# Performance work log

Measured on AMD Instinct MI355X. Metric: run time of the kernel, lower is better.

## Reference

```python
import jax, jax.numpy as jnp
import numpy as np

DN = ('NCHW', 'OIHW', 'NCHW')
BLOB_HW = 16  # hard-coded in make_gaussian_blob_maps

_ENC = [(32, 3), (32, 32), (64, 32), (64, 64), (128, 64), (128, 128), (128, 128)]
_DEC = [(64, 128), (64, 64), (32, 64), (32, 32), (16, 32), (16, 16)]


def _conv(x, w, b, stride):
    y = jax.lax.conv_general_dilated(x, w, (stride, stride), 'SAME', dimension_numbers=DN)
    return y + b[None, :, None, None]


def _tconv(x, w, b):
    # decoder stride-2 stage: 'iteratively doubling the input width'
    y = jax.lax.conv_transpose(x, w, (2, 2), 'SAME', dimension_numbers=DN)
    return y + b[None, :, None, None]


def setup_inputs() -> dict:
    key = jax.random.key(0)
    keys = jax.random.split(key, 1 + 2 * (len(_ENC) + len(_DEC)))
    inp = {'x': jax.random.normal(keys[0], (4, 8, 3, 128, 128), jnp.float32)}
    i = 1
    for j, (o, c) in enumerate(_ENC):
        inp[f'enc_w{j}'] = 0.05 * jax.random.normal(keys[i], (o, c, 3, 3), jnp.float32); i += 1
        inp[f'enc_b{j}'] = 0.05 * jax.random.normal(keys[i], (o,), jnp.float32); i += 1
    for j, (o, c) in enumerate(_DEC):
        inp[f'dec_w{j}'] = 0.05 * jax.random.normal(keys[i], (o, c, 3, 3), jnp.float32); i += 1
        inp[f'dec_b{j}'] = 0.05 * jax.random.normal(keys[i], (o,), jnp.float32); i += 1
    return inp


def _forward(x, enc_w0, enc_b0, enc_w1, enc_b1, enc_w2, enc_b2, enc_w3, enc_b3,
             enc_w4, enc_b4, enc_w5, enc_b5, enc_w6, enc_b6,
             dec_w0, dec_b0, dec_w1, dec_b1, dec_w2, dec_b2,
             dec_w3, dec_b3, dec_w4, dec_b4, dec_w5, dec_b5):
    N, T = x.shape[0], x.shape[1]
    xi = x.reshape((N * T,) + x.shape[2:])  # (B, 3, 128, 128)
    # ---- encoder ----
    h = _conv(xi, enc_w0, enc_b0, 1)                              # Identity act
    h = _conv(h, enc_w1, enc_b1, 1)                               # Identity act
    h = jax.nn.leaky_relu(_conv(h, enc_w2, enc_b2, 2), 0.2)       # 128 -> 64
    h = jax.nn.leaky_relu(_conv(h, enc_w3, enc_b3, 1), 0.2)
    h = jax.nn.leaky_relu(_conv(h, enc_w4, enc_b4, 2), 0.2)       # 64 -> 32
    h = jax.nn.leaky_relu(_conv(h, enc_w5, enc_b5, 1), 0.2)
    R = jax.nn.softplus(_conv(h, enc_w6, enc_b6, 2))              # (B, K, 16, 16)
    B, K, H, W = R.shape
    # ---- keypoint presence: mean over spatial dims ----
    mu = R.sum((2, 3)) / (H * W)                                  # (B, K)
    # ---- normalize_feature_maps: faithful net effect of the in-place loop,
    # which ends up dividing each batch item by the ORIGINAL sum of its LAST map ----
    denom = R[:, K - 1].sum((1, 2))                               # (B,)
    D = R / denom[:, None, None, None]
    # ---- average_feature_maps: spatial-index weighted sum (soft-argmax) ----
    gh = jnp.arange(H, dtype=R.dtype)
    gw = jnp.arange(W, dtype=R.dtype)
    c0 = jnp.einsum('bkhw,h->bk', D, gh)                          # row coord
    c1 = jnp.einsum('bkhw,w->bk', D, gw)                          # col coord
    # ---- gaussian blob maps: mu * exp(-0.5 * ||(u,v) - c||^2), sigma = 1 ----
    u = jnp.arange(BLOB_HW, dtype=R.dtype)[:, None]               # (16, 1)
    v = jnp.arange(BLOB_HW, dtype=R.dtype)[None, :]               # (1, 16)
    d2 = (u[None, None] - c0[:, :, None, None]) ** 2 + (v[None, None] - c1[:, :, None, None]) ** 2
    maps = mu[:, :, None, None] * jnp.exp(-0.5 * d2)              # (B, K, 16, 16)
    # ---- decoder ----
    g = jax.nn.relu(_tconv(maps, dec_w0, dec_b0))                 # 16 -> 32
    g = jax.nn.relu(_conv(g, dec_w1, dec_b1, 1))
    g = jax.nn.relu(_tconv(g, dec_w2, dec_b2))                    # 32 -> 64
    g = jax.nn.relu(_conv(g, dec_w3, dec_b3, 1))
    g = jax.nn.relu(_tconv(g, dec_w4, dec_b4))                    # 64 -> 128
    g = jax.nn.relu(_conv(g, dec_w5, dec_b5, 1))
    return g  # original forward returns the un-reshaped (N*T, C, H, W) tensor


def reference(x, enc_w0, enc_b0, enc_w1, enc_b1, enc_w2, enc_b2, enc_w3, enc_b3,
              enc_w4, enc_b4, enc_w5, enc_b5, enc_w6, enc_b6,
              dec_w0, dec_b0, dec_w1, dec_b1, dec_w2, dec_b2,
              dec_w3, dec_b3, dec_w4, dec_b4, dec_w5, dec_b5):
    return _forward(x, enc_w0, enc_b0, enc_w1, enc_b1, enc_w2, enc_b2, enc_w3, enc_b3,
                    enc_w4, enc_b4, enc_w5, enc_b5, enc_w6, enc_b6,
                    dec_w0, dec_b0, dec_w1, dec_b1, dec_w2, dec_b2,
                    dec_w3, dec_b3, dec_w4, dec_b4, dec_w5, dec_b5)
```

## Files before the change

### kernel.cpp

```cpp
#include <hip/hip_runtime.h>
#include <math.h>


enum { ACT_ID = 0, ACT_LRELU = 1, ACT_SOFTPLUS = 2, ACT_RELU = 3 };

template<int ACT>
__device__ __forceinline__ float act_fn(float x) {
  if (ACT == ACT_LRELU)    return x >= 0.f ? x : 0.2f * x;
  if (ACT == ACT_SOFTPLUS) return fmaxf(x, 0.f) + log1pf(expf(-fabsf(x)));
  if (ACT == ACT_RELU)     return fmaxf(x, 0.f);
  return x;
}

template<int ACT, int NC, int CPT, int CIN>
__global__ __launch_bounds__(256)
void conv_s1(const float* __restrict__ in, const float* __restrict__ w,
             const float* __restrict__ bias, float* __restrict__ out,
             int Cout, int H, int W) {
  const int cogs = Cout / NC;
  const int gx  = blockIdx.x;
  const int cog = gx % cogs;
  const int b   = gx / cogs;
  const int co0 = cog * NC;
  const int Wq  = W / CPT;
  const int items = H * Wq;
  const int item  = blockIdx.y * 256 + threadIdx.x;
  if (item >= items) return;
  const int y  = item / Wq;
  const int x0 = (item - y * Wq) * CPT;

  const int HW = H * W;
  const float* ib = in + (size_t)b * CIN * HW;

  const bool okT = (y > 0), okB = (y < H - 1);
  const bool okL = (x0 > 0), okR = (x0 + CPT < W);
  const int ym = okT ? (y - 1) : 0;
  const int yp = okB ? (y + 1) : 0;
  const int xl = okL ? (x0 - 1) : 0;
  const int xr = okR ? (x0 + CPT) : 0;

  float acc[NC][CPT];
  #pragma unroll
  for (int u = 0; u < NC; ++u)
    #pragma unroll
    for (int q = 0; q < CPT; ++q) acc[u][q] = 0.f;

  #pragma unroll 2
  for (int ci = 0; ci < CIN; ++ci) {
    const float* p = ib + ci * HW;
    const float* wci = w + ((size_t)co0 * CIN + ci) * 9;
    #pragma unroll
    for (int dy = 0; dy < 3; ++dy) {
      const int  ry    = (dy == 0) ? ym : ((dy == 1) ? y : yp);
      const bool okRow = (dy == 0) ? okT : ((dy == 1) ? true : okB);
      const float* r = p + ry * W;
      float v[CPT + 2];
      if (CPT == 4) {
        float  lf = r[xl];
        float4 m  = *(const float4*)(r + x0);
        float  rf = r[xr];
        v[0] = (okRow && okL) ? lf : 0.f;
        v[1] = okRow ? m.x : 0.f;
        v[2] = okRow ? m.y : 0.f;
        v[3] = okRow ? m.z : 0.f;
        v[4] = okRow ? m.w : 0.f;
        v[5] = (okRow && okR) ? rf : 0.f;
      } else if (CPT == 2) {
        float  lf = r[xl];
        float2 m  = *(const float2*)(r + x0);
        float  rf = r[xr];
        v[0] = (okRow && okL) ? lf : 0.f;
        v[1] = okRow ? m.x : 0.f;
        v[2] = okRow ? m.y : 0.f;
        v[3] = (okRow && okR) ? rf : 0.f;
      } else {
        v[0] = (okRow && okL) ? r[xl] : 0.f;
        #pragma unroll
        for (int q = 0; q < CPT; ++q) v[1 + q] = okRow ? r[x0 + q] : 0.f;
        v[CPT + 1] = (okRow && okR) ? r[xr] : 0.f;
      }
      #pragma unroll
      for (int u = 0; u < NC; ++u) {
        const float* wp = wci + u * CIN * 9 + dy * 3;
        const float w0 = wp[0], w1 = wp[1], w2 = wp[2];
        #pragma unroll
        for (int q = 0; q < CPT; ++q)
          acc[u][q] += v[q] * w0 + v[q + 1] * w1 + v[q + 2] * w2;
      }
    }
  }

  #pragma unroll
  for (int u = 0; u < NC; ++u) {
    const float bv = bias[co0 + u];
    float* op = out + ((size_t)(b * Cout + co0 + u) * H + y) * W + x0;
    if (CPT == 4) {
      float4 r4;
      r4.x = act_fn<ACT>(acc[u][0] + bv);
      r4.y = act_fn<ACT>(acc[u][1] + bv);
      r4.z = act_fn<ACT>(acc[u][2] + bv);
      r4.w = act_fn<ACT>(acc[u][3] + bv);
      *(float4*)op = r4;
    } else if (CPT == 2) {
      float2 r2;
      r2.x = act_fn<ACT>(acc[u][0] + bv);
      r2.y = act_fn<ACT>(acc[u][1] + bv);
      *(float2*)op = r2;
    } else {
      #pragma unroll
      for (int q = 0; q < CPT; ++q) op[q] = act_fn<ACT>(acc[u][q] + bv);
    }
  }
}

template<int ACT, int NC, int CPT, int CIN>
__global__ __launch_bounds__(256)
void conv_s2(const float* __restrict__ in, const float* __restrict__ w,
             const float* __restrict__ bias, float* __restrict__ out,
             int Cout, int H, int W) {
  const int Ho = H >> 1, Wo = W >> 1;
  const int cogs = Cout / NC;
  const int gx  = blockIdx.x;
  const int cog = gx % cogs;
  const int b   = gx / cogs;
  const int co0 = cog * NC;
  const int Wq  = Wo / CPT;
  const int items = Ho * Wq;
  const int item  = blockIdx.y * 256 + threadIdx.x;
  if (item >= items) return;
  const int y  = item / Wq;
  const int x0 = (item - y * Wq) * CPT;
  const int ix = 2 * x0;

  const int HW = H * W;
  const float* ib = in + (size_t)b * CIN * HW;

  const int iy0 = 2 * y, iy1 = 2 * y + 1, iy2 = 2 * y + 2;
  const bool okB = (iy2 < H);
  const int iy2c = okB ? iy2 : 0;
  const bool okR = (ix + 2 * CPT < W);
  const int ixr  = okR ? (ix + 2 * CPT) : 0;

  float acc[NC][CPT];
  #pragma unroll
  for (int u = 0; u < NC; ++u)
    #pragma unroll
    for (int q = 0; q < CPT; ++q) acc[u][q] = 0.f;

  #pragma unroll 2
  for (int ci = 0; ci < CIN; ++ci) {
    const float* p = ib + ci * HW;
    const float* wci = w + ((size_t)co0 * CIN + ci) * 9;
    #pragma unroll
    for (int dy = 0; dy < 3; ++dy) {
      const int  ry    = (dy == 0) ? iy0 : ((dy == 1) ? iy1 : iy2c);
      const bool okRow = (dy < 2) || okB;
      const float* r = p + ry * W;
      float v[2 * CPT + 1];
      if (CPT == 4) {
        float4 m0 = *(const float4*)(r + ix);
        float4 m1 = *(const float4*)(r + ix + 4);
        float  rf = r[ixr];
        v[0] = okRow ? m0.x : 0.f; v[1] = okRow ? m0.y : 0.f;
        v[2] = okRow ? m0.z : 0.f; v[3] = okRow ? m0.w : 0.f;
        v[4] = okRow ? m1.x : 0.f; v[5] = okRow ? m1.y : 0.f;
        v[6] = okRow ? m1.z : 0.f; v[7] = okRow ? m1.w : 0.f;
        v[8] = (okRow && okR) ? rf : 0.f;
      } else if (CPT == 2) {
        float4 m0 = *(const float4*)(r + ix);
        float  rf = r[ixr];
        v[0] = okRow ? m0.x : 0.f; v[1] = okRow ? m0.y : 0.f;
        v[2] = okRow ? m0.z : 0.f; v[3] = okRow ? m0.w : 0.f;
        v[4] = (okRow && okR) ? rf : 0.f;
      } else if (CPT == 1) {
        float2 m0 = *(const float2*)(r + ix);
        float  rf = r[ixr];
        v[0] = okRow ? m0.x : 0.f; v[1] = okRow ? m0.y : 0.f;
        v[2] = (okRow && okR) ? rf : 0.f;
      } else {
        #pragma unroll
        for (int q = 0; q < 2 * CPT; ++q) v[q] = okRow ? r[ix + q] : 0.f;
        v[2 * CPT] = (okRow && okR) ? r[ixr] : 0.f;
      }
      #pragma unroll
      for (int u = 0; u < NC; ++u) {
        const float* wp = wci + u * CIN * 9 + dy * 3;
        const float w0 = wp[0], w1 = wp[1], w2 = wp[2];
        #pragma unroll
        for (int q = 0; q < CPT; ++q)
          acc[u][q] += v[2*q] * w0 + v[2*q + 1] * w1 + v[2*q + 2] * w2;
      }
    }
  }

  #pragma unroll
  for (int u = 0; u < NC; ++u) {
    const float bv = bias[co0 + u];
    float* op = out + ((size_t)(b * Cout + co0 + u) * Ho + y) * Wo + x0;
    if (CPT == 4) {
      float4 r4;
      r4.x = act_fn<ACT>(acc[u][0] + bv);
      r4.y = act_fn<ACT>(acc[u][1] + bv);
      r4.z = act_fn<ACT>(acc[u][2] + bv);
      r4.w = act_fn<ACT>(acc[u][3] + bv);
      *(float4*)op = r4;
    } else if (CPT == 2) {
      float2 r2;
      r2.x = act_fn<ACT>(acc[u][0] + bv);
      r2.y = act_fn<ACT>(acc[u][1] + bv);
      *(float2*)op = r2;
    } else {
      #pragma unroll
      for (int q = 0; q < CPT; ++q) op[q] = act_fn<ACT>(acc[u][q] + bv);
    }
  }
}

template<int ACT, int NC, int CIN>
__global__ __launch_bounds__(256)
void tconv(const float* __restrict__ in, const float* __restrict__ w,
           const float* __restrict__ bias, float* __restrict__ out,
           int Cout, int Hin) {
  const int cogs = Cout / NC;
  const int gx  = blockIdx.x;
  const int cog = gx % cogs;
  const int b   = gx / cogs;
  const int co0 = cog * NC;
  const int items = Hin * Hin;
  const int item  = blockIdx.y * 256 + threadIdx.x;
  if (item >= items) return;
  const int i = item / Hin;
  const int j = item - i * Hin;

  const float* ib = in + (size_t)b * CIN * items;
  const bool okT = (i > 0), okL = (j > 0);
  const int im = okT ? i - 1 : 0;
  const int jm = okL ? j - 1 : 0;

  float a00[NC], a01[NC], a10[NC], a11[NC];
  #pragma unroll
  for (int u = 0; u < NC; ++u) { a00[u]=0.f; a01[u]=0.f; a10[u]=0.f; a11[u]=0.f; }

  #pragma unroll 4
  for (int ci = 0; ci < CIN; ++ci) {
    const float* p = ib + ci * items;
    float xtl = p[im*Hin + jm]; xtl = (okT && okL) ? xtl : 0.f;
    float xtr = p[im*Hin + j];  xtr = okT ? xtr : 0.f;
    float xbl = p[i*Hin + jm];  xbl = okL ? xbl : 0.f;
    float xbr = p[i*Hin + j];
    const float* wci = w + ((size_t)co0 * CIN + ci) * 9;
    #pragma unroll
    for (int u = 0; u < NC; ++u) {
      const float* wp = wci + u * CIN * 9;
      const float w00 = wp[0], w01 = wp[1], w02 = wp[2];
      const float w10 = wp[3], w11 = wp[4], w12 = wp[5];
      const float w20 = wp[6], w21 = wp[7], w22 = wp[8];
      a00[u] += xtl*w00 + xtr*w02 + xbl*w20 + xbr*w22;
      a01[u] += xtr*w01 + xbr*w21;
      a10[u] += xbl*w10 + xbr*w12;
      a11[u] += xbr*w11;
    }
  }

  const int Ho = Hin * 2;
  #pragma unroll
  for (int u = 0; u < NC; ++u) {
    const float bv = bias[co0 + u];
    float* op = out + (size_t)(b * Cout + co0 + u) * Ho * Ho + (2*i) * Ho + 2*j;
    float2 t0, t1;
    t0.x = act_fn<ACT>(a00[u] + bv); t0.y = act_fn<ACT>(a01[u] + bv);
    t1.x = act_fn<ACT>(a10[u] + bv); t1.y = act_fn<ACT>(a11[u] + bv);
    *(float2*)op = t0;
    *(float2*)(op + Ho) = t1;
  }
}

__global__ __launch_bounds__(64)
void kp_reduce(const float* __restrict__ R, float* __restrict__ S,
               float* __restrict__ Sh, float* __restrict__ Sw) {
  const int bk = blockIdx.x;
  const int t = threadIdx.x;
  const float* p = R + (size_t)bk * 256;
  float s = 0.f, sh = 0.f, sw = 0.f;
  #pragma unroll
  for (int q = 0; q < 4; ++q) {
    int idx = t + q * 64;
    float v = p[idx];
    s  += v;
    sh += v * (float)(idx >> 4);
    sw += v * (float)(idx & 15);
  }
  #pragma unroll
  for (int off = 32; off > 0; off >>= 1) {
    s  += __shfl_down(s, off);
    sh += __shfl_down(sh, off);
    sw += __shfl_down(sw, off);
  }
  if (t == 0) { S[bk] = s; Sh[bk] = sh; Sw[bk] = sw; }
}

__global__ __launch_bounds__(256)
void kp_maps(const float* __restrict__ S, const float* __restrict__ Sh,
             const float* __restrict__ Sw, float* __restrict__ maps, int K) {
  const int bk = blockIdx.x;
  const int b = bk / K;
  const int t = threadIdx.x;
  const float s   = S[bk];
  const float den = S[b * K + (K - 1)];
  const float mu  = s * (1.0f / 256.0f);
  const float c0  = Sh[bk] / den;
  const float c1  = Sw[bk] / den;
  const float u = (float)(t >> 4);
  const float v = (float)(t & 15);
  const float d2 = (u - c0) * (u - c0) + (v - c1) * (v - c1);
  maps[(size_t)bk * 256 + t] = mu * expf(-0.5f * d2);
}

extern "C" void kernel_launch(void* const* d_in, const int* in_sizes, int n_in,
                              void* d_out, int out_size, void* d_ws, size_t ws_size,
                              hipStream_t stream) {
  const int B = 32;
  const float* x = (const float*)d_in[0];
  const float* ew[7]; const float* eb[7];
  for (int j = 0; j < 7; ++j) { ew[j] = (const float*)d_in[1 + 2*j]; eb[j] = (const float*)d_in[2 + 2*j]; }
  const float* dw[6]; const float* db[6];
  for (int j = 0; j < 6; ++j) { dw[j] = (const float*)d_in[15 + 2*j]; db[j] = (const float*)d_in[16 + 2*j]; }

  float* ws   = (float*)d_ws;
  float* bufA = ws;
  float* bufB = bufA + 16777216;
  float* R    = bufB + 16777216;
  float* maps = R + 1048576;
  float* S    = maps + 1048576;
  float* Sh   = S + 4096;
  float* Sw   = Sh + 4096;
  float* outp = (float*)d_out;

  dim3 blk(256);

  conv_s1<ACT_ID,      8,4,3>  <<<dim3(B*4,  16), blk, 0, stream>>>(x,    ew[0], eb[0], bufA, 32,  128, 128);
  conv_s1<ACT_ID,      8,4,32> <<<dim3(B*4,  16), blk, 0, stream>>>(bufA, ew[1], eb[1], bufB, 32,  128, 128);
  conv_s2<ACT_LRELU,   8,4,32> <<<dim3(B*8,   4), blk, 0, stream>>>(bufB, ew[2], eb[2], bufA, 64,  128, 128);
  conv_s1<ACT_LRELU,   8,4,64> <<<dim3(B*8,   4), blk, 0, stream>>>(bufA, ew[3], eb[3], bufB, 64,  64,  64);
  conv_s2<ACT_LRELU,   8,2,64> <<<dim3(B*16,  2), blk, 0, stream>>>(bufB, ew[4], eb[4], bufA, 128, 64,  64);
  conv_s1<ACT_LRELU,   8,2,128><<<dim3(B*16,  2), blk, 0, stream>>>(bufA, ew[5], eb[5], bufB, 128, 32,  32);
  conv_s2<ACT_SOFTPLUS,4,1,128><<<dim3(B*32,  1), blk, 0, stream>>>(bufB, ew[6], eb[6], R,    128, 32,  32);

  kp_reduce<<<dim3(B*128), dim3(64), 0, stream>>>(R, S, Sh, Sw);
  kp_maps  <<<dim3(B*128), blk, 0, stream>>>(S, Sh, Sw, maps, 128);

  tconv<ACT_RELU,   2,128><<<dim3(B*32,  1), blk, 0, stream>>>(maps, dw[0], db[0], bufA, 64, 16);
  conv_s1<ACT_RELU, 4,2,64><<<dim3(B*16,  2), blk, 0, stream>>>(bufA, dw[1], db[1], bufB, 64, 32, 32);
  tconv<ACT_RELU,   4,64> <<<dim3(B*8,   4), blk, 0, stream>>>(bufB, dw[2], db[2], bufA, 32, 32);
  conv_s1<ACT_RELU, 8,2,32><<<dim3(B*4,   8), blk, 0, stream>>>(bufA, dw[3], db[3], bufB, 32, 64, 64);
  tconv<ACT_RELU,   8,32> <<<dim3(B*2,  16), blk, 0, stream>>>(bufB, dw[4], db[4], bufA, 16, 64);
  conv_s1<ACT_RELU, 8,4,16><<<dim3(B*2,  16), blk, 0, stream>>>(bufA, dw[5], db[5], outp, 16, 128, 128);
}
```

Before: 1.301 ms.

## Compute two output rows per thread in stride-1 convs to reuse input rows

Adds a conv_s1r2 kernel in which each thread produces two adjacent output rows. It loads four input rows per channel instead of three per output row, cutting input loads per output and reusing each loaded row for both outputs. Most stride-1 convs switch to it, several with fewer output channels per block (8 to 4) to keep register pressure and grid size in check. The tconv channel-loop unroll also drops from 4 to 2, and unused CPT branches are removed from the older kernels.

```diff
diff --git a/kernel.cpp b/kernel.cpp
--- a/kernel.cpp
+++ b/kernel.cpp
@@ -10,6 +10,121 @@
   if (ACT == ACT_SOFTPLUS) return fmaxf(x, 0.f) + log1pf(expf(-fabsf(x)));
   if (ACT == ACT_RELU)     return fmaxf(x, 0.f);
   return x;
+}
+
+template<int ACT, int NC, int CPT, int CIN>
+__global__ __launch_bounds__(256)
+void conv_s1r2(const float* __restrict__ in, const float* __restrict__ w,
+               const float* __restrict__ bias, float* __restrict__ out,
+               int Cout, int H, int W) {
+  const int cogs = Cout / NC;
+  const int gx  = blockIdx.x;
+  const int cog = gx % cogs;
+  const int b   = gx / cogs;
+  const int co0 = cog * NC;
+  const int Wq  = W / CPT;
+  const int Hp  = H >> 1;
+  const int items = Hp * Wq;
+  const int item  = blockIdx.y * 256 + threadIdx.x;
+  if (item >= items) return;
+  const int yp = item / Wq;
+  const int x0 = (item - yp * Wq) * CPT;
+  const int y0 = 2 * yp;
+
+  const int HW = H * W;
+  const float* ib = in + (size_t)b * CIN * HW;
+
+  const bool okT = (y0 > 0), okB = (y0 + 2 < H);
+  const bool okL = (x0 > 0), okR = (x0 + CPT < W);
+  const int xl = okL ? (x0 - 1) : 0;
+  const int xr = okR ? (x0 + CPT) : 0;
+
+  float acc[NC][2][CPT];
+  #pragma unroll
+  for (int u = 0; u < NC; ++u)
+    #pragma unroll
+    for (int o = 0; o < 2; ++o)
+      #pragma unroll
+      for (int q = 0; q < CPT; ++q) acc[u][o][q] = 0.f;
+
+  #pragma unroll 1
+  for (int ci = 0; ci < CIN; ++ci) {
+    const float* p = ib + ci * HW;
+    const float* wci = w + ((size_t)co0 * CIN + ci) * 9;
+    #pragma unroll
+    for (int r = 0; r < 4; ++r) {
+      const bool ok = (r == 0) ? okT : ((r == 3) ? okB : true);
+      const int iy = ok ? (y0 - 1 + r) : 0;
+      const float* row = p + iy * W;
+      float v[CPT + 2];
+      if (CPT == 4) {
+        float  lf = row[xl];
+        float4 m  = *(const float4*)(row + x0);
+        float  rf = row[xr];
+        v[0] = (ok && okL) ? lf : 0.f;
+        v[1] = ok ? m.x : 0.f;
+        v[2] = ok ? m.y : 0.f;
+        v[3] = ok ? m.z : 0.f;
+        v[4] = ok ? m.w : 0.f;
+        v[5] = (ok && okR) ? rf : 0.f;
+      } else if (CPT == 2) {
+        float  lf = row[xl];
+        float2 m  = *(const float2*)(row + x0);
+        float  rf = row[xr];
+        v[0] = (ok && okL) ? lf : 0.f;
+        v[1] = ok ? m.x : 0.f;
+        v[2] = ok ? m.y : 0.f;
+        v[3] = (ok && okR) ? rf : 0.f;
+      } else {
+        v[0] = (ok && okL) ? row[xl] : 0.f;
+        #pragma unroll
+        for (int q = 0; q < CPT; ++q) v[1 + q] = ok ? row[x0 + q] : 0.f;
+        v[CPT + 1] = (ok && okR) ? row[xr] : 0.f;
+      }
+      #pragma unroll
+      for (int u = 0; u < NC; ++u) {
+        const float* wp = wci + (size_t)u * CIN * 9;
+        if (r <= 2) {
+          const float w0 = wp[r * 3], w1 = wp[r * 3 + 1], w2 = wp[r * 3 + 2];
+          #pragma unroll
+          for (int q = 0; q < CPT; ++q)
+            acc[u][0][q] += v[q] * w0 + v[q + 1] * w1 + v[q + 2] * w2;
+        }
+        if (r >= 1) {
+          const float w0 = wp[(r-1) * 3], w1 = wp[(r-1) * 3 + 1], w2 = wp[(r-1) * 3 + 2];
+          #pragma unroll
+          for (int q = 0; q < CPT; ++q)
+            acc[u][1][q] += v[q] * w0 + v[q + 1] * w1 + v[q + 2] * w2;
+        }
+      }
+    }
+  }
+
+  #pragma unroll
+  for (int u = 0; u < NC; ++u) {
+    const float bv = bias[co0 + u];
+    float* op = out + ((size_t)(b * Cout + co0 + u) * H + y0) * W + x0;
+    #pragma unroll
+    for (int o = 0; o < 2; ++o) {
+      float* opo = op + o * W;
+      if (CPT == 4) {
+        float4 r4;
+        r4.x = act_fn<ACT>(acc[u][o][0] + bv);
+        r4.y = act_fn<ACT>(acc[u][o][1] + bv);
+        r4.z = act_fn<ACT>(acc[u][o][2] + bv);
+        r4.w = act_fn<ACT>(acc[u][o][3] + bv);
+        *(float4*)opo = r4;
+      } else if (CPT == 2) {
+        float2 r2;
+        r2.x = act_fn<ACT>(acc[u][o][0] + bv);
+        r2.y = act_fn<ACT>(acc[u][o][1] + bv);
+        *(float2*)opo = r2;
+      } else {
+        #pragma unroll
+        for (int q = 0; q < CPT; ++q) opo[q] = act_fn<ACT>(acc[u][o][q] + bv);
+      }
+    }
+  }
 }
 
 template<int ACT, int NC, int CPT, int CIN>
@@ -55,17 +170,7 @@
       const bool okRow = (dy == 0) ? okT : ((dy == 1) ? true : okB);
       const float* r = p + ry * W;
       float v[CPT + 2];
-      if (CPT == 4) {
-        float  lf = r[xl];
-        float4 m  = *(const float4*)(r + x0);
-        float  rf = r[xr];
-        v[0] = (okRow && okL) ? lf : 0.f;
-        v[1] = okRow ? m.x : 0.f;
-        v[2] = okRow ? m.y : 0.f;
-        v[3] = okRow ? m.z : 0.f;
-        v[4] = okRow ? m.w : 0.f;
-        v[5] = (okRow && okR) ? rf : 0.f;
-      } else if (CPT == 2) {
+      if (CPT == 2) {
         float  lf = r[xl];
         float2 m  = *(const float2*)(r + x0);
         float  rf = r[xr];
@@ -94,14 +199,7 @@
   for (int u = 0; u < NC; ++u) {
     const float bv = bias[co0 + u];
     float* op = out + ((size_t)(b * Cout + co0 + u) * H + y) * W + x0;
-    if (CPT == 4) {
-      float4 r4;
-      r4.x = act_fn<ACT>(acc[u][0] + bv);
-      r4.y = act_fn<ACT>(acc[u][1] + bv);
-      r4.z = act_fn<ACT>(acc[u][2] + bv);
-      r4.w = act_fn<ACT>(acc[u][3] + bv);
-      *(float4*)op = r4;
-    } else if (CPT == 2) {
+    if (CPT == 2) {
       float2 r2;
       r2.x = act_fn<ACT>(acc[u][0] + bv);
       r2.y = act_fn<ACT>(acc[u][1] + bv);
@@ -172,15 +270,11 @@
         v[0] = okRow ? m0.x : 0.f; v[1] = okRow ? m0.y : 0.f;
         v[2] = okRow ? m0.z : 0.f; v[3] = okRow ? m0.w : 0.f;
         v[4] = (okRow && okR) ? rf : 0.f;
-      } else if (CPT == 1) {
+      } else {
         float2 m0 = *(const float2*)(r + ix);
         float  rf = r[ixr];
         v[0] = okRow ? m0.x : 0.f; v[1] = okRow ? m0.y : 0.f;
         v[2] = (okRow && okR) ? rf : 0.f;
-      } else {
-        #pragma unroll
-        for (int q = 0; q < 2 * CPT; ++q) v[q] = okRow ? r[ix + q] : 0.f;
-        v[2 * CPT] = (okRow && okR) ? r[ixr] : 0.f;
       }
       #pragma unroll
       for (int u = 0; u < NC; ++u) {
@@ -241,7 +335,7 @@
   #pragma unroll
   for (int u = 0; u < NC; ++u) { a00[u]=0.f; a01[u]=0.f; a10[u]=0.f; a11[u]=0.f; }
 
-  #pragma unroll 4
+  #pragma unroll 2
   for (int ci = 0; ci < CIN; ++ci) {
     const float* p = ib + ci * items;
     float xtl = p[im*Hin + jm]; xtl = (okT && okL) ? xtl : 0.f;
@@ -338,21 +432,21 @@
 
   dim3 blk(256);
 
-  conv_s1<ACT_ID,      8,4,3>  <<<dim3(B*4,  16), blk, 0, stream>>>(x,    ew[0], eb[0], bufA, 32,  128, 128);
-  conv_s1<ACT_ID,      8,4,32> <<<dim3(B*4,  16), blk, 0, stream>>>(bufA, ew[1], eb[1], bufB, 32,  128, 128);
+  conv_s1r2<ACT_ID,    8,4,3>  <<<dim3(B*4,   8), blk, 0, stream>>>(x,    ew[0], eb[0], bufA, 32,  128, 128);
+  conv_s1r2<ACT_ID,    8,4,32> <<<dim3(B*4,   8), blk, 0, stream>>>(bufA, ew[1], eb[1], bufB, 32,  128, 128);
   conv_s2<ACT_LRELU,   8,4,32> <<<dim3(B*8,   4), blk, 0, stream>>>(bufB, ew[2], eb[2], bufA, 64,  128, 128);
-  conv_s1<ACT_LRELU,   8,4,64> <<<dim3(B*8,   4), blk, 0, stream>>>(bufA, ew[3], eb[3], bufB, 64,  64,  64);
+  conv_s1r2<ACT_LRELU, 4,4,64> <<<dim3(B*16,  2), blk, 0, stream>>>(bufA, ew[3], eb[3], bufB, 64,  64,  64);
   conv_s2<ACT_LRELU,   8,2,64> <<<dim3(B*16,  2), blk, 0, stream>>>(bufB, ew[4], eb[4], bufA, 128, 64,  64);
-  conv_s1<ACT_LRELU,   8,2,128><<<dim3(B*16,  2), blk, 0, stream>>>(bufA, ew[5], eb[5], bufB, 128, 32,  32);
+  conv_s1r2<ACT_LRELU, 4,2,128><<<dim3(B*32,  1), blk, 0, stream>>>(bufA, ew[5], eb[5], bufB, 128, 32,  32);
   conv_s2<ACT_SOFTPLUS,4,1,128><<<dim3(B*32,  1), blk, 0, stream>>>(bufB, ew[6], eb[6], R,    128, 32,  32);
 
   kp_reduce<<<dim3(B*128), dim3(64), 0, stream>>>(R, S, Sh, Sw);
   kp_maps  <<<dim3(B*128), blk, 0, stream>>>(S, Sh, Sw, maps, 128);
 
-  tconv<ACT_RELU,   2,128><<<dim3(B*32,  1), blk, 0, stream>>>(maps, dw[0], db[0], bufA, 64, 16);
+  tconv<ACT_RELU,   2,128> <<<dim3(B*32,  1), blk, 0, stream>>>(maps, dw[0], db[0], bufA, 64, 16);
   conv_s1<ACT_RELU, 4,2,64><<<dim3(B*16,  2), blk, 0, stream>>>(bufA, dw[1], db[1], bufB, 64, 32, 32);
-  tconv<ACT_RELU,   4,64> <<<dim3(B*8,   4), blk, 0, stream>>>(bufB, dw[2], db[2], bufA, 32, 32);
-  conv_s1<ACT_RELU, 8,2,32><<<dim3(B*4,   8), blk, 0, stream>>>(bufA, dw[3], db[3], bufB, 32, 64, 64);
-  tconv<ACT_RELU,   8,32> <<<dim3(B*2,  16), blk, 0, stream>>>(bufB, dw[4], db[4], bufA, 16, 64);
-  conv_s1<ACT_RELU, 8,4,16><<<dim3(B*2,  16), blk, 0, stream>>>(bufA, dw[5], db[5], outp, 16, 128, 128);
-}
+  tconv<ACT_RELU,   4,64>  <<<dim3(B*8,   4), blk, 0, stream>>>(bufB, dw[2], db[2], bufA, 32, 32);
+  conv_s1r2<ACT_RELU,4,2,32><<<dim3(B*8,   4), blk, 0, stream>>>(bufA, dw[3], db[3], bufB, 32, 64, 64);
+  tconv<ACT_RELU,   8,32>  <<<dim3(B*2,  16), blk, 0, stream>>>(bufB, dw[4], db[4], bufA, 16, 64);
+  conv_s1r2<ACT_RELU,4,4,16><<<dim3(B*4,   8), blk, 0, stream>>>(bufA, dw[5], db[5], outp, 16, 128, 128);
+}
```

After: 1.207 ms. 1.08x faster.
